# Performance work log

Hardware: AMD Instinct MI355X
Metric: run time of the kernel (lower is better)

## Reference

```python
import jax, jax.numpy as jnp
from jax import lax
import numpy as np

D_MODEL = 1024
EXPAND = 2
D_INNER = EXPAND * D_MODEL      # 2048
D_STATE = 16
D_CONV = 4
DT_RANK = (D_MODEL + 15) // 16  # 64 ('auto')


def setup_inputs() -> dict:
    key = jax.random.key(0)
    ks = jax.random.split(key, 20)
    B, L = 2, 1024
    inp = {
        "x": jax.random.normal(ks[0], (B, L, D_MODEL), jnp.float32),
        "input_mask": jnp.ones((B, L, 1), jnp.float32),
        # shared projections (BiMambaBlock ties in_proj/out_proj between directions)
        "in_proj_w": jax.random.normal(ks[1], (2 * D_INNER, D_MODEL), jnp.float32) * (D_MODEL ** -0.5),
        "out_proj_w": jax.random.normal(ks[2], (D_MODEL, D_INNER), jnp.float32) * (D_INNER ** -0.5),
    }
    for tag, off in (("f", 3), ("r", 11)):
        inp[f"conv_w_{tag}"] = jax.random.normal(ks[off], (D_INNER, 1, D_CONV), jnp.float32) * (D_CONV ** -0.5)
        inp[f"conv_b_{tag}"] = jax.random.normal(ks[off + 1], (D_INNER,), jnp.float32) * 0.01
        inp[f"x_proj_w_{tag}"] = jax.random.normal(ks[off + 2], (DT_RANK + 2 * D_STATE, D_INNER), jnp.float32) * (D_INNER ** -0.5)
        inp[f"dt_w_{tag}"] = jax.random.normal(ks[off + 3], (D_INNER, DT_RANK), jnp.float32) * (DT_RANK ** -0.5)
        # dt bias ~ inverse-softplus of dt in [dt_min, dt_max]
        dt = jnp.exp(jax.random.uniform(ks[off + 4], (D_INNER,)) * (np.log(0.1) - np.log(0.001)) + np.log(0.001))
        inp[f"dt_b_{tag}"] = dt + jnp.log(-jnp.expm1(-dt))
        # A = -exp(A_log), A_log init = log(1..d_state)
        inp[f"A_log_{tag}"] = jnp.log(jnp.broadcast_to(jnp.arange(1, D_STATE + 1, dtype=jnp.float32), (D_INNER, D_STATE)))
        inp[f"D_{tag}"] = jnp.ones((D_INNER,), jnp.float32)
    return inp


def _mamba(x, in_proj_w, conv_w, conv_b, x_proj_w, dt_w, dt_b, A_log, D, out_proj_w):
    B, L, _ = x.shape
    xz = x @ in_proj_w.T                         # (B, L, 2*d_inner)
    u, z = jnp.split(xz, 2, axis=-1)             # each (B, L, d_inner)
    # depthwise causal conv over sequence
    uc = jnp.transpose(u, (0, 2, 1))             # (B, d_inner, L)
    uc = lax.conv_general_dilated(uc, conv_w, (1,), [(D_CONV - 1, 0)],
                                  feature_group_count=D_INNER) + conv_b[None, :, None]
    u = jax.nn.silu(jnp.transpose(uc, (0, 2, 1)))  # (B, L, d_inner)
    x_dbl = u @ x_proj_w.T                         # (B, L, dt_rank + 2*d_state)
    dt, Bs, Cs = jnp.split(x_dbl, [DT_RANK, DT_RANK + D_STATE], axis=-1)
    delta = jax.nn.softplus(dt @ dt_w.T + dt_b)    # (B, L, d_inner)
    A = -jnp.exp(A_log)                            # (d_inner, d_state)
    dA = jnp.exp(delta[..., None] * A)             # (B, L, d_inner, d_state)
    dBu = delta[..., None] * Bs[:, :, None, :] * u[..., None]

    def step(h, t):
        dA_t, dBu_t, C_t = t
        h = dA_t * h + dBu_t                       # (B, d_inner, d_state)
        y = jnp.einsum('bds,bs->bd', h, C_t)
        return h, y

    h0 = jnp.zeros((B, D_INNER, D_STATE), x.dtype)
    _, ys = lax.scan(step, h0, (jnp.moveaxis(dA, 1, 0), jnp.moveaxis(dBu, 1, 0), jnp.moveaxis(Cs, 1, 0)))
    y = jnp.moveaxis(ys, 0, 1) + u * D             # (B, L, d_inner)
    y = y * jax.nn.silu(z)
    return y @ out_proj_w.T                        # (B, L, d_model)


def reference(x, input_mask, in_proj_w, out_proj_w,
              conv_w_f, conv_b_f, x_proj_w_f, dt_w_f, dt_b_f, A_log_f, D_f,
              conv_w_r, conv_b_r, x_proj_w_r, dt_w_r, dt_b_r, A_log_r, D_r):
    x = x * input_mask
    y_fwd = _mamba(x, in_proj_w, conv_w_f, conv_b_f, x_proj_w_f, dt_w_f, dt_b_f, A_log_f, D_f, out_proj_w)
    # NOTE: original flips dims=[-1] -> the FEATURE axis (faithful reproduction)
    y_rev = _mamba(jnp.flip(x, axis=-1), in_proj_w, conv_w_r, conv_b_r, x_proj_w_r, dt_w_r, dt_b_r, A_log_r, D_r, out_proj_w)
    return y_fwd + y_rev
```

## Files before the change

kernel.cpp:

```cpp
#include <hip/hip_runtime.h>

#define DM   1024
#define DI   2048
#define DS   16
#define RK   64
#define NBAT 2
#define LL   1024
#define MR   (NBAT*LL)
#define NCH  128
#define LC   (LL/NCH)

typedef short  bf16x8 __attribute__((ext_vector_type(8)));
typedef short  short8v __attribute__((ext_vector_type(8)));
typedef float  f32x4  __attribute__((ext_vector_type(4)));

__device__ __forceinline__ float bf2f(unsigned short u) {
  union { unsigned int i; float f; } v; v.i = ((unsigned int)u) << 16; return v.f;
}
__device__ __forceinline__ unsigned short f2bf(float f) {
  union { float f; unsigned int i; } v; v.f = f;
  return (unsigned short)((v.i + 0x7FFFu + ((v.i >> 16) & 1u)) >> 16);
}
__device__ __forceinline__ float fsilu(float z) {
  return z * __builtin_amdgcn_rcpf(1.f + __expf(-z));
}
__device__ __forceinline__ float fsoftplus(float x) {
  return fmaxf(x, 0.f) + __logf(1.f + __expf(-fabsf(x)));
}

#define N_XB    (MR*DM)
#define N_WH    (4096*1024)
#define N_XPB   (96*DI)
#define N_DTWB  (DI*RK)
#define N_OPB   (DM*DI)
#define N_A2    (DI*DS)
#define N_ZXD   (2*MR*96)
#define N_ZOUT  (MR*DM)
#define N_PREP  (N_XB + N_WH + 2*N_XPB + 2*N_DTWB + N_OPB + 2*N_A2 + N_ZXD + N_ZOUT)

__device__ __forceinline__ void cvt4(const float* src, unsigned short* dst) {
  const float4 v = *(const float4*)src;
  ushort4 o; o.x = f2bf(v.x); o.y = f2bf(v.y); o.z = f2bf(v.z); o.w = f2bf(v.w);
  *(ushort4*)dst = o;
}

__global__ void prep_all(const float* __restrict__ x, const float* __restrict__ mask,
                         const float* __restrict__ W,
                         const float* __restrict__ xpw_f, const float* __restrict__ xpw_r,
                         const float* __restrict__ dtw_f, const float* __restrict__ dtw_r,
                         const float* __restrict__ outpw,
                         const float* __restrict__ Af, const float* __restrict__ Ar,
                         unsigned short* __restrict__ xb, unsigned short* __restrict__ Wcat,
                         unsigned short* __restrict__ xpb, unsigned short* __restrict__ dtwb,
                         unsigned short* __restrict__ opb, float* __restrict__ A2,
                         float* __restrict__ xdbl_z, float* __restrict__ out_z)
{
  int i = (blockIdx.x * 256 + threadIdx.x) * 4;
  if (i < N_XB) {
    const float4 v = *(const float4*)&x[i];
    const float m = mask[i >> 10];
    ushort4 o; o.x = f2bf(v.x * m); o.y = f2bf(v.y * m); o.z = f2bf(v.z * m); o.w = f2bf(v.w * m);
    *(ushort4*)&xb[i] = o; return;
  }
  i -= N_XB;
  if (i < N_WH) {
    const int nrow = i >> 10, k = i & 1023;
    const float4 v = *(const float4*)&W[i];
    ushort4 o; o.x = f2bf(v.x); o.y = f2bf(v.y); o.z = f2bf(v.z); o.w = f2bf(v.w);
    *(ushort4*)&Wcat[i] = o;
    ushort4 rr; rr.x = f2bf(v.w); rr.y = f2bf(v.z); rr.z = f2bf(v.y); rr.w = f2bf(v.x);
    *(ushort4*)&Wcat[(size_t)(4096 + nrow) * 1024 + (1020 - k)] = rr;
    return;
  }
  i -= N_WH;
  if (i < N_XPB) { cvt4(&xpw_f[i], &xpb[i]); return; }
  i -= N_XPB;
  if (i < N_XPB) { cvt4(&xpw_r[i], &xpb[N_XPB + i]); return; }
  i -= N_XPB;
  if (i < N_DTWB) { cvt4(&dtw_f[i], &dtwb[i]); return; }
  i -= N_DTWB;
  if (i < N_DTWB) { cvt4(&dtw_r[i], &dtwb[N_DTWB + i]); return; }
  i -= N_DTWB;
  if (i < N_OPB) { cvt4(&outpw[i], &opb[i]); return; }
  i -= N_OPB;
  if (i < N_A2) {
    const float4 v = *(const float4*)&Af[i];
    float4 o; o.x = -__expf(v.x); o.y = -__expf(v.y); o.z = -__expf(v.z); o.w = -__expf(v.w);
    *(float4*)&A2[i] = o; return;
  }
  i -= N_A2;
  if (i < N_A2) {
    const float4 v = *(const float4*)&Ar[i];
    float4 o; o.x = -__expf(v.x); o.y = -__expf(v.y); o.z = -__expf(v.z); o.w = -__expf(v.w);
    *(float4*)&A2[N_A2 + i] = o; return;
  }
  i -= N_A2;
  if (i < N_ZXD) { *(float4*)&xdbl_z[i] = (float4){0.f, 0.f, 0.f, 0.f}; return; }
  i -= N_ZXD;
  if (i < N_ZOUT) { *(float4*)&out_z[i] = (float4){0.f, 0.f, 0.f, 0.f}; return; }
}

__global__ void cvt_dtb(const float* __restrict__ xdbl, unsigned short* __restrict__ dtb) {
  int i = (blockIdx.x * 256 + threadIdx.x) * 4;
  if (i < 2 * MR * RK) {
    const int dir = i / (MR * RK);
    const int j = i % (MR * RK);
    const int r = j >> 6, k = j & 63;
    cvt4(&xdbl[(size_t)dir * (MR * 96) + (size_t)r * 96 + k], &dtb[i]);
  }
}

__global__ __launch_bounds__(512)
void gemm256(const unsigned short* __restrict__ A, const unsigned short* __restrict__ B,
             unsigned short* __restrict__ C)
{
  __shared__ __align__(16) unsigned short As[2][16384];
  __shared__ __align__(16) unsigned short Bs[2][16384];
  const int tid = threadIdx.x;
  const int wid = tid >> 6, lane = tid & 63;
  const int bm = blockIdx.y * 256;
  const int bn = blockIdx.x * 256;
  const int wm = wid >> 2, wn = wid & 3;
  const bool isA = wid < 4;
  const int cw = isA ? wid : wid - 4;

  const unsigned short* sp[8];
#pragma unroll
  for (int l = 0; l < 8; ++l) {
    const int row = cw * 64 + l * 8 + (lane >> 3);
    const int col = ((lane & 7) * 8) ^ (((row >> 1) & 7) << 3);
    sp[l] = (isA ? A + (size_t)(bm + row) * 1024
                 : B + (size_t)(bn + row) * 1024) + col;
  }
  const int dbase = cw * 4096 + lane * 8;

  f32x4 acc[8][4];
#pragma unroll
  for (int rf = 0; rf < 8; ++rf)
#pragma unroll
    for (int cf = 0; cf < 4; ++cf) acc[rf][cf] = (f32x4){0.f, 0.f, 0.f, 0.f};

#define STG256(b, kt)                                                                  \
  do {                                                                                 \
    unsigned short* dst = (isA ? &As[b][0] : &Bs[b][0]) + dbase;                       \
    const int kk = (kt) * 64;                                                          \
    _Pragma("unroll")                                                                  \
    for (int l = 0; l < 8; ++l)                                                        \
      __builtin_amdgcn_global_load_lds(                                                \
          (const __attribute__((address_space(1))) void*)(sp[l] + kk),                 \
          (__attribute__((address_space(3))) void*)(dst + l * 512), 16, 0, 0);         \
  } while (0)

  const int rsel = lane & 15;
  const int ko = (lane >> 4) * 8;
  const int swzl = ((rsel >> 1) & 7) << 3;

  STG256(0, 0);
  __syncthreads();
  for (int t = 0; t < 16; ++t) {
    const int buf = t & 1;
    if (t < 15) STG256(buf ^ 1, t + 1);
    const unsigned short* pa = &As[buf][0];
    const unsigned short* pb = &Bs[buf][0];
#pragma unroll
    for (int ks = 0; ks < 2; ++ks) {
      const int kl = (ks * 32 + ko) ^ swzl;
      bf16x8 bfv[4];
#pragma unroll
      for (int cf = 0; cf < 4; ++cf)
        bfv[cf] = *(const bf16x8*)&pb[(wn * 64 + cf * 16 + rsel) * 64 + kl];
#pragma unroll
      for (int rf = 0; rf < 8; ++rf) {
        const bf16x8 af = *(const bf16x8*)&pa[(wm * 128 + rf * 16 + rsel) * 64 + kl];
#pragma unroll
        for (int cf = 0; cf < 4; ++cf)
          acc[rf][cf] = __builtin_amdgcn_mfma_f32_16x16x32_bf16(af, bfv[cf], acc[rf][cf], 0, 0, 0);
      }
    }
    __syncthreads();
  }
#undef STG256

#pragma unroll
  for (int rf = 0; rf < 8; ++rf) {
    const int row0 = bm + wm * 128 + rf * 16 + (lane >> 4) * 4;
#pragma unroll
    for (int cf = 0; cf < 4; ++cf) {
      const int col = bn + wn * 64 + cf * 16 + rsel;
#pragma unroll
      for (int j = 0; j < 4; ++j)
        C[(size_t)(row0 + j) * 8192 + col] = f2bf(acc[rf][cf][j]);
    }
  }
}

struct GArg { const unsigned short* A; const unsigned short* B; void* C; const float* bias; };

template<int EPI, int OUT, int ATOMIC, int NDIR>
__global__ __launch_bounds__(256)
void gemm_bt(GArg g0, GArg g1, int M, int N, int K, int lda, int ldb, int ldc, int koff)
{
  __shared__ __align__(16) unsigned short As[2][128 * 32];
  __shared__ __align__(16) unsigned short Bs[2][128 * 32];
  const GArg ga = (NDIR == 2 && (blockIdx.z & 1)) ? g1 : g0;
  const int kc = (NDIR == 2) ? ((int)blockIdx.z >> 1) : (int)blockIdx.z;
  const unsigned short* Ap = ga.A + (size_t)kc * koff;
  const unsigned short* Bp = ga.B + (size_t)kc * koff;

  const int tid  = threadIdx.x;
  const int wave = tid >> 6;
  const int lane = tid & 63;
  const int bm = blockIdx.y * 128;
  const int bn = blockIdx.x * 128;
  const int wr = wave >> 1, wc = wave & 1;

  f32x4 acc[4][4];
#pragma unroll
  for (int m = 0; m < 4; ++m)
#pragma unroll
    for (int n = 0; n < 4; ++n) acc[m][n] = (f32x4){0.f, 0.f, 0.f, 0.f};

  const int rsel = lane & 15;
  const int ksel = (lane >> 4) * 8;
  const int NT = K >> 5;

  const int chunk0 = wave * 2;
  const int flat0  = chunk0 * 512 + lane * 8;
  const int row0s  = flat0 >> 5, col0s = flat0 & 31;
  const int flat1  = (chunk0 + 1) * 512 + lane * 8;
  const int row1s  = flat1 >> 5, col1s = flat1 & 31;
  int grA0 = bm + row0s; if (grA0 > M - 1) grA0 = M - 1;
  int grA1 = bm + row1s; if (grA1 > M - 1) grA1 = M - 1;
  int gcB0 = bn + row0s; if (gcB0 > N - 1) gcB0 = N - 1;
  int gcB1 = bn + row1s; if (gcB1 > N - 1) gcB1 = N - 1;

#define STAGE(buf, kt)                                                                       \
  do {                                                                                       \
    const int k0_ = (kt) << 5;                                                               \
    __builtin_amdgcn_global_load_lds(                                                        \
        (const __attribute__((address_space(1))) void*)(Ap + (size_t)grA0 * lda + k0_ + col0s), \
        (__attribute__((address_space(3))) void*)(&As[buf][chunk0 * 512]), 16, 0, 0);        \
    __builtin_amdgcn_global_load_lds(                                                        \
        (const __attribute__((address_space(1))) void*)(Ap + (size_t)grA1 * lda + k0_ + col1s), \
        (__attribute__((address_space(3))) void*)(&As[buf][(chunk0 + 1) * 512]), 16, 0, 0);  \
    __builtin_amdgcn_global_load_lds(                                                        \
        (const __attribute__((address_space(1))) void*)(Bp + (size_t)gcB0 * ldb + k0_ + col0s), \
        (__attribute__((address_space(3))) void*)(&Bs[buf][chunk0 * 512]), 16, 0, 0);        \
    __builtin_amdgcn_global_load_lds(                                                        \
        (const __attribute__((address_space(1))) void*)(Bp + (size_t)gcB1 * ldb + k0_ + col1s), \
        (__attribute__((address_space(3))) void*)(&Bs[buf][(chunk0 + 1) * 512]), 16, 0, 0);  \
  } while (0)

  STAGE(0, 0);
  __syncthreads();
  int cur = 0;
  for (int kt = 0; kt < NT; ++kt) {
    if (kt + 1 < NT) STAGE(cur ^ 1, kt + 1);
    bf16x8 af[4], bfv[4];
#pragma unroll
    for (int m = 0; m < 4; ++m)
      af[m] = *(const bf16x8*)&As[cur][(wr * 64 + m * 16 + rsel) * 32 + ksel];
#pragma unroll
    for (int n = 0; n < 4; ++n)
      bfv[n] = *(const bf16x8*)&Bs[cur][(wc * 64 + n * 16 + rsel) * 32 + ksel];
#pragma unroll
    for (int m = 0; m < 4; ++m)
#pragma unroll
      for (int n = 0; n < 4; ++n)
        acc[m][n] = __builtin_amdgcn_mfma_f32_16x16x32_bf16(af[m], bfv[n], acc[m][n], 0, 0, 0);
    if (kt + 1 < NT) {
      __syncthreads();
      cur ^= 1;
    }
  }
#undef STAGE

#pragma unroll
  for (int m = 0; m < 4; ++m) {
    const int rowb = bm + wr * 64 + m * 16 + (lane >> 4) * 4;
#pragma unroll
    for (int n = 0; n < 4; ++n) {
      const int col = bn + wc * 64 + n * 16 + rsel;
      if (col < N) {
#pragma unroll
        for (int r = 0; r < 4; ++r) {
          const int rr = rowb + r;
          if (rr < M) {
            float v = acc[m][n][r];
            if constexpr (EPI == 1) {
              v = fsoftplus(v + ga.bias[col]);
            }
            if constexpr (ATOMIC) {
              atomicAdd((float*)ga.C + (size_t)rr * ldc + col, v);
            } else if constexpr (OUT == 1) {
              ((unsigned short*)ga.C)[(size_t)rr * ldc + col] = f2bf(v);
            } else {
              ((float*)ga.C)[(size_t)rr * ldc + col] = v;
            }
          }
        }
      }
    }
  }
}

__global__ __launch_bounds__(256)
void conv_silu_k(const unsigned short* __restrict__ xz,
                 const float* __restrict__ cw_f, const float* __restrict__ cb_f,
                 const float* __restrict__ cw_r, const float* __restrict__ cb_r,
                 unsigned short* __restrict__ ub)
{
  const int tid = threadIdx.x;
  const int d0  = tid * 8;
  const int l0  = blockIdx.x * 8;
  const int dir = blockIdx.y >> 1, b = blockIdx.y & 1;
  const float* cw = dir ? cw_r : cw_f;
  const float* cb = dir ? cb_r : cb_f;
  float w0[8], w1[8], w2[8], w3[8], bs[8];
#pragma unroll
  for (int j = 0; j < 8; ++j) {
    const float4 wv = *(const float4*)&cw[(d0 + j) * 4];
    w0[j] = wv.x; w1[j] = wv.y; w2[j] = wv.z; w3[j] = wv.w;
    bs[j] = cb[d0 + j];
  }
  const unsigned short* uin = xz + (size_t)dir * 4096 + d0;
  unsigned short* uo = ub + (size_t)dir * ((size_t)MR * DI) + d0;
  const size_t rbase = (size_t)b * LL;
  float xa[8], xbv[8], xc[8];
#pragma unroll
  for (int j = 0; j < 8; ++j) { xa[j] = 0.f; xbv[j] = 0.f; xc[j] = 0.f; }
  if (l0 >= 3) { const short8v v = *(const short8v*)&uin[(rbase + l0 - 3) * 8192];
#pragma unroll
    for (int j = 0; j < 8; ++j) xa[j] = bf2f((unsigned short)v[j]); }
  if (l0 >= 2) { const short8v v = *(const short8v*)&uin[(rbase + l0 - 2) * 8192];
#pragma unroll
    for (int j = 0; j < 8; ++j) xbv[j] = bf2f((unsigned short)v[j]); }
  if (l0 >= 1) { const short8v v = *(const short8v*)&uin[(rbase + l0 - 1) * 8192];
#pragma unroll
    for (int j = 0; j < 8; ++j) xc[j] = bf2f((unsigned short)v[j]); }
  for (int l = l0; l < l0 + 8; ++l) {
    const short8v v = *(const short8v*)&uin[(rbase + l) * 8192];
    short8v ov;
#pragma unroll
    for (int j = 0; j < 8; ++j) {
      const float x3 = bf2f((unsigned short)v[j]);
      float o = w0[j] * xa[j] + w1[j] * xbv[j] + w2[j] * xc[j] + w3[j] * x3 + bs[j];
      ov[j] = (short)f2bf(fsilu(o));
      xa[j] = xbv[j]; xbv[j] = xc[j]; xc[j] = x3;
    }
    *(short8v*)&uo[(rbase + l) * DI] = ov;
  }
}

__global__ __launch_bounds__(256)
void scanA(const unsigned short* __restrict__ dlt, const unsigned short* __restrict__ ub,
           const float* __restrict__ xdbl, const float* __restrict__ A2,
           float* __restrict__ sdl, unsigned short* __restrict__ hb)
{
  const int tid = threadIdx.x;
  const int d = blockIdx.x * 256 + tid;
  const int c = blockIdx.y;
  const int dir = blockIdx.z >> 1, b = blockIdx.z & 1;
  __shared__ float sB[LC * DS];
  const float* xd = xdbl + (size_t)dir * (MR * 96);
  for (int i = tid; i < LC * DS; i += 256) {
    int t = i >> 4, s = i & 15;
    sB[i] = xd[(size_t)(b * LL + c * LC + t) * 96 + 64 + s];
  }
  __syncthreads();
  const unsigned short* dl_p = dlt + (size_t)dir * ((size_t)MR * DI) + d;
  const unsigned short* uu = ub + (size_t)dir * ((size_t)MR * DI) + d;
  float a2[DS];
#pragma unroll
  for (int s = 0; s < DS; ++s) a2[s] = A2[((size_t)dir * DI + d) * DS + s];
  float h[DS];
#pragma unroll
  for (int s = 0; s < DS; ++s) h[s] = 0.f;
  float sumdl = 0.f;
  for (int t = 0; t < LC; ++t) {
    size_t r = (size_t)b * LL + c * LC + t;
    float dl = bf2f(dl_p[r * DI]);
    float du = dl * bf2f(uu[r * DI]);
    sumdl += dl;
#pragma unroll
    for (int s = 0; s < DS; ++s) {
      float e = __expf(dl * a2[s]);
      h[s] = e * h[s] + du * sB[t * DS + s];
    }
  }
  const size_t base = ((((size_t)(dir * 2 + b)) * NCH + c) * DI + d) * DS;
#pragma unroll
  for (int s = 0; s < DS; ++s) hb[base + s] = f2bf(h[s]);
  sdl[(((size_t)(dir * 2 + b)) * NCH + c) * DI + d] = sumdl;
}

__global__ __launch_bounds__(256)
void scanB(const float* __restrict__ sdl, const float* __restrict__ A2,
           unsigned short* __restrict__ hb)
{
  const int i = blockIdx.x * 256 + threadIdx.x;
  const int db = i >> 15;
  const int ds_ = i & 32767;
  const int d = ds_ >> 4, s = i & 15;
  const int dir = db >> 1;
  const float a2 = A2[((size_t)dir * DI + d) * DS + s];
  float hrun = 0.f;
  for (int c = 0; c < NCH; ++c) {
    const size_t off = (((size_t)db * NCH + c) << 15) + ds_;
    const float h0 = bf2f(hb[off]);
    const float pa = __expf(a2 * sdl[((size_t)db * NCH + c) * DI + d]);
    hb[off] = f2bf(hrun);
    hrun = pa * hrun + h0;
  }
}

__global__ __launch_bounds__(512)
void scanC_f(const unsigned short* __restrict__ xz, const unsigned short* __restrict__ ub,
             const unsigned short* __restrict__ dlt, const float* __restrict__ xdbl,
             const float* __restrict__ A2, const float* __restrict__ Dv_f,
             const float* __restrict__ Dv_r, const unsigned short* __restrict__ hb,
             unsigned short* __restrict__ ygb)
{
  const int tid = threadIdx.x;
  const int dir = tid >> 8;
  const int td  = tid & 255;
  const int d = blockIdx.x * 256 + td;
  const int c = blockIdx.y;
  const int b = blockIdx.z;
  __shared__ float sB[2][LC * DS], sC[2][LC * DS];
  __shared__ float sY[LC][256];
  for (int i = tid; i < 2 * LC * DS; i += 512) {
    const int di = i >> 7;
    const int j = i & 127;
    const int t = j >> 4, s = j & 15;
    const size_t ro = (size_t)di * (MR * 96) + (size_t)(b * LL + c * LC + t) * 96;
    sB[di][j] = xdbl[ro + 64 + s];
    sC[di][j] = xdbl[ro + 80 + s];
  }
  __syncthreads();
  float a2[DS], h[DS];
  const size_t base = ((((size_t)(dir * 2 + b)) * NCH + c) * DI + d) * DS;
#pragma unroll
  for (int s = 0; s < DS; ++s) {
    a2[s] = A2[((size_t)dir * DI + d) * DS + s];
    h[s] = bf2f(hb[base + s]);
  }
  const float Dd = dir ? Dv_r[d] : Dv_f[d];
  const unsigned short* dl_p = dlt + (size_t)dir * ((size_t)MR * DI) + d;
  const unsigned short* uu  = ub + (size_t)dir * ((size_t)MR * DI) + d;
  float yg[LC];
#pragma unroll
  for (int t = 0; t < LC; ++t) {
    const size_t r = (size_t)b * LL + c * LC + t;
    const float dl = bf2f(dl_p[r * DI]);
    const float uf = bf2f(uu[r * DI]);
    const float du = dl * uf;
    float y = 0.f;
#pragma unroll
    for (int s = 0; s < DS; ++s) {
      const float e = __expf(dl * a2[s]);
      h[s] = e * h[s] + du * sB[dir][t * DS + s];
      y += h[s] * sC[dir][t * DS + s];
    }
    y += Dd * uf;
    const float z = bf2f(xz[r * 8192 + 2048 + dir * 4096 + d]);
    yg[t] = y * fsilu(z);
  }
  if (dir == 1) {
#pragma unroll
    for (int t = 0; t < LC; ++t) sY[t][td] = yg[t];
  }
  __syncthreads();
  if (dir == 0) {
#pragma unroll
    for (int t = 0; t < LC; ++t) {
      const size_t r = (size_t)b * LL + c * LC + t;
      ygb[r * DI + d] = f2bf(yg[t] + sY[t][td]);
    }
  }
}


extern "C" void kernel_launch(void* const* d_in, const int* in_sizes, int n_in,
                              void* d_out, int out_size, void* d_ws, size_t ws_size,
                              hipStream_t stream)
{
  (void)in_sizes; (void)n_in; (void)out_size; (void)ws_size;
  const float* x      = (const float*)d_in[0];
  const float* mask   = (const float*)d_in[1];
  const float* inpw   = (const float*)d_in[2];
  const float* outpw  = (const float*)d_in[3];
  const float* cw_f   = (const float*)d_in[4];
  const float* cb_f   = (const float*)d_in[5];
  const float* xpw_f  = (const float*)d_in[6];
  const float* dtw_f  = (const float*)d_in[7];
  const float* dtbias_f = (const float*)d_in[8];
  const float* alog_f = (const float*)d_in[9];
  const float* Dv_f   = (const float*)d_in[10];
  const float* cw_r   = (const float*)d_in[11];
  const float* cb_r   = (const float*)d_in[12];
  const float* xpw_r  = (const float*)d_in[13];
  const float* dtw_r  = (const float*)d_in[14];
  const float* dtbias_r = (const float*)d_in[15];
  const float* alog_r = (const float*)d_in[16];
  const float* Dv_r   = (const float*)d_in[17];
  float* out = (float*)d_out;

  char* p = (char*)d_ws;
  auto carve = [&](size_t bytes) -> char* {
    char* q = p; p += (bytes + 255) & ~(size_t)255; return q;
  };
  unsigned short* xb   = (unsigned short*)carve((size_t)MR * DM * 2);
  unsigned short* Wcat = (unsigned short*)carve((size_t)8192 * 1024 * 2);
  unsigned short* xpb  = (unsigned short*)carve((size_t)2 * 96 * DI * 2);
  unsigned short* dtwb = (unsigned short*)carve((size_t)2 * DI * RK * 2);
  unsigned short* opb  = (unsigned short*)carve((size_t)DM * DI * 2);
  float*          A2   = (float*)carve((size_t)2 * DI * DS * 4);
  unsigned short* xz   = (unsigned short*)carve((size_t)MR * 8192 * 2);
  unsigned short* dlt  = (unsigned short*)carve((size_t)2 * MR * DI * 2);
  unsigned short* ub   = (unsigned short*)carve((size_t)2 * MR * DI * 2);
  float*          xdbl = (float*)carve((size_t)2 * MR * 96 * 4);
  unsigned short* dtb  = (unsigned short*)carve((size_t)2 * MR * RK * 2);
  float*          sdl  = (float*)carve((size_t)4 * NCH * DI * 4);
  unsigned short* hb   = (unsigned short*)carve((size_t)4 * NCH * DI * DS * 2);
  unsigned short* ygb  = (unsigned short*)carve((size_t)MR * DI * 2);

  prep_all<<<(N_PREP / 4 + 255) / 256, 256, 0, stream>>>(
      x, mask, inpw, xpw_f, xpw_r, dtw_f, dtw_r, outpw, alog_f, alog_r,
      xb, Wcat, xpb, dtwb, opb, A2, xdbl, out);

  gemm256<<<dim3(32, 8, 1), 512, 0, stream>>>(xb, Wcat, xz);

  conv_silu_k<<<dim3(128, 4, 1), 256, 0, stream>>>(xz, cw_f, cb_f, cw_r, cb_r, ub);
  {
    GArg g0{ub, xpb, xdbl, nullptr};
    GArg g1{ub + (size_t)MR * DI, xpb + 96 * DI, xdbl + (size_t)MR * 96, nullptr};
    gemm_bt<0, 0, 1, 2><<<dim3(1, 16, 16), 256, 0, stream>>>(
        g0, g1, MR, 96, 256, DI, DI, 96, 256);
  }
  cvt_dtb<<<(2 * MR * RK / 4 + 255) / 256, 256, 0, stream>>>(xdbl, dtb);
  {
    GArg g0{dtb, dtwb, dlt, dtbias_f};
    GArg g1{dtb + (size_t)MR * RK, dtwb + DI * RK, dlt + (size_t)MR * DI, dtbias_r};
    gemm_bt<1, 1, 0, 2><<<dim3(16, 16, 2), 256, 0, stream>>>(
        g0, g1, MR, DI, 64, RK, RK, DI, 0);
  }
  scanA<<<dim3(8, NCH, 4), 256, 0, stream>>>(dlt, ub, xdbl, A2, sdl, hb);
  scanB<<<dim3(512, 1, 1), 256, 0, stream>>>(sdl, A2, hb);
  scanC_f<<<dim3(8, NCH, 2), 512, 0, stream>>>(xz, ub, dlt, xdbl, A2, Dv_f, Dv_r, hb, ygb);
  {
    GArg g0{ygb, opb, out, nullptr};
    gemm_bt<0, 0, 1, 1><<<dim3(8, 16, 4), 256, 0, stream>>>(
        g0, g0, MR, DM, 512, DI, DI, DM, 512);
  }
}
```

Measured before the change: 212.6 us.

## Replace atomic split-K accumulation with partial buffers and reduction kernels

The split-K GEMMs for x_proj and out_proj no longer atomically add into zeroed fp32 outputs. Each K-slice now writes its own partial buffer, and new reduction kernels sum them. The x_proj reduction also emits the bf16 dt input, so the separate conversion kernel and the zero-fill in prep go away. The out_proj split drops from 4 to 2 slices and reuses the Wcat buffer for partials, which removes atomic contention at the cost of an extra reduction pass and less parallelism in the final GEMM.

```diff
diff --git a/kernel.cpp b/kernel.cpp
--- a/kernel.cpp
+++ b/kernel.cpp
@@ -34,9 +34,7 @@
 #define N_DTWB  (DI*RK)
 #define N_OPB   (DM*DI)
 #define N_A2    (DI*DS)
-#define N_ZXD   (2*MR*96)
-#define N_ZOUT  (MR*DM)
-#define N_PREP  (N_XB + N_WH + 2*N_XPB + 2*N_DTWB + N_OPB + 2*N_A2 + N_ZXD + N_ZOUT)
+#define N_PREP  (N_XB + N_WH + 2*N_XPB + 2*N_DTWB + N_OPB + 2*N_A2)
 
 __device__ __forceinline__ void cvt4(const float* src, unsigned short* dst) {
   const float4 v = *(const float4*)src;
@@ -52,8 +50,7 @@
                          const float* __restrict__ Af, const float* __restrict__ Ar,
                          unsigned short* __restrict__ xb, unsigned short* __restrict__ Wcat,
                          unsigned short* __restrict__ xpb, unsigned short* __restrict__ dtwb,
-                         unsigned short* __restrict__ opb, float* __restrict__ A2,
-                         float* __restrict__ xdbl_z, float* __restrict__ out_z)
+                         unsigned short* __restrict__ opb, float* __restrict__ A2)
 {
   int i = (blockIdx.x * 256 + threadIdx.x) * 4;
   if (i < N_XB) {
@@ -94,20 +91,6 @@
     float4 o; o.x = -__expf(v.x); o.y = -__expf(v.y); o.z = -__expf(v.z); o.w = -__expf(v.w);
     *(float4*)&A2[N_A2 + i] = o; return;
   }
-  i -= N_A2;
-  if (i < N_ZXD) { *(float4*)&xdbl_z[i] = (float4){0.f, 0.f, 0.f, 0.f}; return; }
-  i -= N_ZXD;
-  if (i < N_ZOUT) { *(float4*)&out_z[i] = (float4){0.f, 0.f, 0.f, 0.f}; return; }
-}
-
-__global__ void cvt_dtb(const float* __restrict__ xdbl, unsigned short* __restrict__ dtb) {
-  int i = (blockIdx.x * 256 + threadIdx.x) * 4;
-  if (i < 2 * MR * RK) {
-    const int dir = i / (MR * RK);
-    const int j = i % (MR * RK);
-    const int r = j >> 6, k = j & 63;
-    cvt4(&xdbl[(size_t)dir * (MR * 96) + (size_t)r * 96 + k], &dtb[i]);
-  }
 }
 
 __global__ __launch_bounds__(512)
@@ -196,9 +179,10 @@
 
 struct GArg { const unsigned short* A; const unsigned short* B; void* C; const float* bias; };
 
-template<int EPI, int OUT, int ATOMIC, int NDIR>
+template<int EPI, int OUT, int NDIR>
 __global__ __launch_bounds__(256)
-void gemm_bt(GArg g0, GArg g1, int M, int N, int K, int lda, int ldb, int ldc, int koff)
+void gemm_bt(GArg g0, GArg g1, int M, int N, int K, int lda, int ldb, int ldc,
+             int koff, int coff)
 {
   __shared__ __align__(16) unsigned short As[2][128 * 32];
   __shared__ __align__(16) unsigned short Bs[2][128 * 32];
@@ -206,6 +190,7 @@
   const int kc = (NDIR == 2) ? ((int)blockIdx.z >> 1) : (int)blockIdx.z;
   const unsigned short* Ap = ga.A + (size_t)kc * koff;
   const unsigned short* Bp = ga.B + (size_t)kc * koff;
+  const size_t cbase = (size_t)kc * coff;
 
   const int tid  = threadIdx.x;
   const int wave = tid >> 6;
@@ -290,17 +275,42 @@
             if constexpr (EPI == 1) {
               v = fsoftplus(v + ga.bias[col]);
             }
-            if constexpr (ATOMIC) {
-              atomicAdd((float*)ga.C + (size_t)rr * ldc + col, v);
-            } else if constexpr (OUT == 1) {
-              ((unsigned short*)ga.C)[(size_t)rr * ldc + col] = f2bf(v);
+            if constexpr (OUT == 1) {
+              ((unsigned short*)ga.C)[cbase + (size_t)rr * ldc + col] = f2bf(v);
             } else {
-              ((float*)ga.C)[(size_t)rr * ldc + col] = v;
+              ((float*)ga.C)[cbase + (size_t)rr * ldc + col] = v;
             }
           }
         }
       }
     }
+  }
+}
+
+__global__ void reduce_xdbl(const float* __restrict__ pxd, float* __restrict__ xdbl,
+                            unsigned short* __restrict__ dtb)
+{
+  const int i = blockIdx.x * 256 + threadIdx.x;
+  if (i >= 2 * MR * 96) return;
+  float s = 0.f;
+#pragma unroll
+  for (int k = 0; k < 8; ++k) s += pxd[(size_t)k * (2 * MR * 96) + i];
+  xdbl[i] = s;
+  const int k = i % 96;
+  if (k < 64) {
+    const int dr = i / 96;
+    dtb[(size_t)dr * 64 + k] = f2bf(s);
+  }
+}
+
+__global__ void reduce_out(const float* __restrict__ pout, float* __restrict__ out)
+{
+  const int i = (blockIdx.x * 256 + threadIdx.x) * 4;
+  if (i < MR * DM) {
+    const float4 a = *(const float4*)&pout[i];
+    const float4 b = *(const float4*)&pout[(size_t)MR * DM + i];
+    float4 o; o.x = a.x + b.x; o.y = a.y + b.y; o.z = a.z + b.z; o.w = a.w + b.w;
+    *(float4*)&out[i] = o;
   }
 }
 
@@ -524,33 +534,36 @@
   float*          sdl  = (float*)carve((size_t)4 * NCH * DI * 4);
   unsigned short* hb   = (unsigned short*)carve((size_t)4 * NCH * DI * DS * 2);
   unsigned short* ygb  = (unsigned short*)carve((size_t)MR * DI * 2);
+  float*          pxd  = (float*)carve((size_t)8 * 2 * MR * 96 * 4);
+  float*          pout = (float*)Wcat;
 
   prep_all<<<(N_PREP / 4 + 255) / 256, 256, 0, stream>>>(
       x, mask, inpw, xpw_f, xpw_r, dtw_f, dtw_r, outpw, alog_f, alog_r,
-      xb, Wcat, xpb, dtwb, opb, A2, xdbl, out);
+      xb, Wcat, xpb, dtwb, opb, A2);
 
   gemm256<<<dim3(32, 8, 1), 512, 0, stream>>>(xb, Wcat, xz);
 
   conv_silu_k<<<dim3(128, 4, 1), 256, 0, stream>>>(xz, cw_f, cb_f, cw_r, cb_r, ub);
   {
-    GArg g0{ub, xpb, xdbl, nullptr};
-    GArg g1{ub + (size_t)MR * DI, xpb + 96 * DI, xdbl + (size_t)MR * 96, nullptr};
-    gemm_bt<0, 0, 1, 2><<<dim3(1, 16, 16), 256, 0, stream>>>(
-        g0, g1, MR, 96, 256, DI, DI, 96, 256);
-  }
-  cvt_dtb<<<(2 * MR * RK / 4 + 255) / 256, 256, 0, stream>>>(xdbl, dtb);
+    GArg g0{ub, xpb, pxd, nullptr};
+    GArg g1{ub + (size_t)MR * DI, xpb + 96 * DI, pxd + (size_t)MR * 96, nullptr};
+    gemm_bt<0, 0, 2><<<dim3(1, 16, 16), 256, 0, stream>>>(
+        g0, g1, MR, 96, 256, DI, DI, 96, 256, 2 * MR * 96);
+  }
+  reduce_xdbl<<<(2 * MR * 96 + 255) / 256, 256, 0, stream>>>(pxd, xdbl, dtb);
   {
     GArg g0{dtb, dtwb, dlt, dtbias_f};
     GArg g1{dtb + (size_t)MR * RK, dtwb + DI * RK, dlt + (size_t)MR * DI, dtbias_r};
-    gemm_bt<1, 1, 0, 2><<<dim3(16, 16, 2), 256, 0, stream>>>(
-        g0, g1, MR, DI, 64, RK, RK, DI, 0);
+    gemm_bt<1, 1, 2><<<dim3(16, 16, 2), 256, 0, stream>>>(
+        g0, g1, MR, DI, 64, RK, RK, DI, 0, 0);
   }
   scanA<<<dim3(8, NCH, 4), 256, 0, stream>>>(dlt, ub, xdbl, A2, sdl, hb);
   scanB<<<dim3(512, 1, 1), 256, 0, stream>>>(sdl, A2, hb);
   scanC_f<<<dim3(8, NCH, 2), 512, 0, stream>>>(xz, ub, dlt, xdbl, A2, Dv_f, Dv_r, hb, ygb);
   {
-    GArg g0{ygb, opb, out, nullptr};
-    gemm_bt<0, 0, 1, 1><<<dim3(8, 16, 4), 256, 0, stream>>>(
-        g0, g0, MR, DM, 512, DI, DI, DM, 512);
-  }
-}
+    GArg g0{ygb, opb, pout, nullptr};
+    gemm_bt<0, 0, 1><<<dim3(8, 16, 2), 256, 0, stream>>>(
+        g0, g0, MR, DM, 1024, DI, DI, DM, 1024, MR * DM);
+  }
+  reduce_out<<<(MR * DM / 4 + 255) / 256, 256, 0, stream>>>(pout, out);
+}
```

New measurement: 199.2 us. 6.3% less time.
